# Kernel optimization log

Hardware: AMD Instinct MI355X
Metric: run time of the kernel (lower is better)

## Reference

```python
import jax, jax.numpy as jnp
import numpy as np
import math

EMBED_DIM = 256
NUM_HEADS = 8
FFN_DIM = 1024
EPS = 1e-5


def layer_norm(x, g, b):
    mu = jnp.mean(x, axis=-1, keepdims=True)
    var = jnp.var(x, axis=-1, keepdims=True)
    return (x - mu) / jnp.sqrt(var + EPS) * g + b


def setup_inputs() -> dict:
    key = jax.random.key(0)
    ks = jax.random.split(key, 10)
    B, L, D, F = 4, 2048, EMBED_DIM, FFN_DIM
    x = jax.random.normal(ks[0], (B, L, D), dtype=jnp.float32)
    mask = jnp.ones((B, L), dtype=jnp.int32)
    # FFN params (PyTorch Linear default-ish scale)
    W1 = jax.random.normal(ks[1], (D, F), dtype=jnp.float32) / np.sqrt(D)
    b1 = jnp.zeros((F,), dtype=jnp.float32)
    W2 = jax.random.normal(ks[2], (F, D), dtype=jnp.float32) / np.sqrt(F)
    b2 = jnp.zeros((D,), dtype=jnp.float32)
    g1 = jnp.ones((D,), dtype=jnp.float32)
    be1 = jnp.zeros((D,), dtype=jnp.float32)
    g2 = jnp.ones((D,), dtype=jnp.float32)
    be2 = jnp.zeros((D,), dtype=jnp.float32)
    return {"x": x, "mask": mask, "W1": W1, "b1": b1, "W2": W2, "b2": b2,
            "g1": g1, "be1": be1, "g2": g2, "be2": be2}


def quantum_attention(x, mask):
    B, L, D = x.shape
    H, dk = NUM_HEADS, D // NUM_HEADS
    xh = x.reshape(B, L, H, dk).transpose(0, 2, 1, 3)  # [B,H,L,dk]
    # per-token mean over batch and heads -> [L, dk]
    m = jnp.mean(xh, axis=(0, 1))
    # closed form of the single-qubit RX circuit: P(|1>) = sin^2(angle/2)
    dot = m @ m.T  # [L, L]
    ang = jnp.clip(dot, -math.pi, math.pi)
    scores = jnp.sin(ang * 0.5) ** 2  # [L, L], shared across B and H
    attn = jnp.broadcast_to(scores[None, None], (B, H, L, L))
    attn = jnp.where(mask[:, None, None, :] == 0, -1e9, attn)
    attn = jax.nn.softmax(attn, axis=-1)
    out = jnp.einsum('bhij,bhjd->bhid', attn, xh)  # values are xh itself
    return out.transpose(0, 2, 1, 3).reshape(B, L, D)


def reference(x, mask, W1, b1, W2, b2, g1, be1, g2, be2):
    attn_out = quantum_attention(x, mask)
    h = layer_norm(x + attn_out, g1, be1)
    ffn = jax.nn.relu(h @ W1 + b1) @ W2 + b2
    return layer_norm(h + ffn, g2, be2)
```

## Files before the change

### kernel.cpp

```cpp
#include <hip/hip_runtime.h>
#include <hip/hip_bf16.h>


#define B_ 4
#define L_ 2048
#define D_ 256
#define F_ 1024
#define PI_F 3.14159265358979323846f

typedef __bf16 bf16x8 __attribute__((ext_vector_type(8)));
typedef float floatx4 __attribute__((ext_vector_type(4)));
typedef unsigned short ushortx4 __attribute__((ext_vector_type(4)));

#define WAIT_VM(n) asm volatile("s_waitcnt vmcnt(" #n ")" ::: "memory")
#define SCHED0() __builtin_amdgcn_sched_barrier(0)
#define BARRIER() do { SCHED0(); __builtin_amdgcn_s_barrier(); SCHED0(); } while (0)

__device__ __forceinline__ unsigned short f2bf(float f) {
    unsigned int u = __float_as_uint(f);
    u = (u + 0x7FFFu + ((u >> 16) & 1u)) >> 16;
    return (unsigned short)u;
}
__device__ __forceinline__ float bf2f(unsigned short u) {
    union { unsigned int i; float f; } v; v.i = ((unsigned int)u) << 16; return v.f;
}

__device__ __forceinline__ void async_cp16(unsigned short* lds, const unsigned short* g) {
    __builtin_amdgcn_global_load_lds(
        (const __attribute__((address_space(1))) unsigned int*)g,
        (__attribute__((address_space(3))) unsigned int*)lds, 16, 0, 0);
}

__global__ __launch_bounds__(256) void k_prep(const float* __restrict__ x,
                                              const float* __restrict__ W1,
                                              const float* __restrict__ W2,
                                              const int* __restrict__ mask,
                                              unsigned short* __restrict__ mb,
                                              unsigned short* __restrict__ XmT,
                                              unsigned short* __restrict__ W1T,
                                              unsigned short* __restrict__ W2T) {
    __shared__ float tile[32][33];
    int r = blockIdx.x, t = threadIdx.x;
    if (r >= 2560) {
        int idx = (r - 2560) * 256 + t;
        int l = idx >> 5, k = idx & 31;
        float s = 0.f;
#pragma unroll
        for (int b = 0; b < B_; b++) {
            const float* xp = x + ((size_t)(b * L_ + l)) * D_ + k;
#pragma unroll
            for (int h = 0; h < 8; h++) s += xp[h * 32];
        }
        mb[idx] = f2bf(s * (1.f / 32.f));
        return;
    }
    const float* in; unsigned short* outp; int R, C; const int* mrow = nullptr; size_t bo = 0;
    int bx, by;
    if (r < 2048) {
        int z = r >> 9, rem = r & 511; by = rem >> 3; bx = rem & 7;
        in = x; outp = XmT; R = L_; C = 256; bo = (size_t)z * R * C; mrow = mask + z * L_;
    } else if (r < 2304) {
        int rem = r - 2048; bx = rem & 31; by = rem >> 5;
        in = W1; outp = W1T; R = 256; C = 1024;
    } else {
        int rem = r - 2304; bx = rem & 7; by = rem >> 3;
        in = W2; outp = W2T; R = 1024; C = 256;
    }
    int r0 = by * 32, c0 = bx * 32;
    int tx = t & 31, ty = t >> 5;
#pragma unroll
    for (int rr = 0; rr < 4; rr++) {
        int rw = ty + rr * 8;
        tile[rw][tx] = in[bo + (size_t)(r0 + rw) * C + c0 + tx];
    }
    float mfac = 1.f;
    if (mrow) mfac = mrow[r0 + tx] ? 1.f : 0.f;
    __syncthreads();
#pragma unroll
    for (int rr = 0; rr < 4; rr++) {
        int c = ty + rr * 8;
        outp[bo + (size_t)(c0 + c) * R + r0 + tx] = f2bf(tile[tx][c] * mfac);
    }
}

__global__ __launch_bounds__(256) void k_scores_mfma(const unsigned short* __restrict__ mb,
                                                     const int* __restrict__ mask,
                                                     unsigned short* __restrict__ E,
                                                     float* __restrict__ rowpart) {
    __shared__ float part[128][2][4];
    const int t = threadIdx.x, lane = t & 63, wid = t >> 6;
    const int wm = (wid >> 1) * 64, wn = (wid & 1) * 32;
    const int lr = lane & 15, lq = lane >> 4;
    int m0 = blockIdx.y * 128, n0 = blockIdx.x * 64;
    bf16x8 af[4], bfr[2];
#pragma unroll
    for (int i = 0; i < 4; i++)
        af[i] = *(const bf16x8*)(mb + (size_t)(m0 + wm + i * 16 + lr) * 32 + lq * 8);
#pragma unroll
    for (int j = 0; j < 2; j++)
        bfr[j] = *(const bf16x8*)(mb + (size_t)(n0 + wn + j * 16 + lr) * 32 + lq * 8);
    floatx4 acc[4][2];
#pragma unroll
    for (int i = 0; i < 4; i++)
#pragma unroll
        for (int j = 0; j < 2; j++) {
            acc[i][j] = (floatx4){0.f, 0.f, 0.f, 0.f};
            acc[i][j] = __builtin_amdgcn_mfma_f32_16x16x32_bf16(af[i], bfr[j], acc[i][j], 0, 0, 0);
        }
    float mv[4][2];
#pragma unroll
    for (int b = 0; b < 4; b++) {
        mv[b][0] = mask[b * L_ + n0 + wn + lr] ? 1.f : 0.f;
        mv[b][1] = mask[b * L_ + n0 + wn + 16 + lr] ? 1.f : 0.f;
    }
#pragma unroll
    for (int i = 0; i < 4; i++) {
#pragma unroll
        for (int j = 0; j < 2; j++)
#pragma unroll
            for (int r = 0; r < 4; r++) {
                int row = m0 + wm + i * 16 + lq * 4 + r;
                int col = n0 + wn + j * 16 + lr;
                float d = fminf(fmaxf(acc[i][j][r], -PI_F), PI_F);
                float sn = __sinf(0.5f * d);
                float e = __expf(sn * sn);
                acc[i][j][r] = e;
                E[(size_t)row * L_ + col] = f2bf(e);
            }
#pragma unroll
        for (int r = 0; r < 4; r++) {
            float pb[4];
#pragma unroll
            for (int b = 0; b < 4; b++)
                pb[b] = acc[i][0][r] * mv[b][0] + acc[i][1][r] * mv[b][1];
#pragma unroll
            for (int o = 1; o < 16; o <<= 1)
#pragma unroll
                for (int b = 0; b < 4; b++) pb[b] += __shfl_xor(pb[b], o);
            if (lr == 0) {
                int lrow = wm + i * 16 + lq * 4 + r;
#pragma unroll
                for (int b = 0; b < 4; b++) part[lrow][wid & 1][b] = pb[b];
            }
        }
    }
    __syncthreads();
    if (t < 128) {
        int grow = m0 + t;
#pragma unroll
        for (int b = 0; b < 4; b++)
            rowpart[((size_t)grow * 4 + b) * 32 + blockIdx.x] = part[t][0][b] + part[t][1][b];
    }
}

__global__ __launch_bounds__(256) void k_av(const unsigned short* __restrict__ E,
                                            const unsigned short* __restrict__ XmT,
                                            unsigned short* __restrict__ Cb) {
    __shared__ __align__(16) unsigned short sbuf[3][128 * 64 + 64 * 64];
    const int t = threadIdx.x, lane = t & 63, wid = t >> 6;
    const int wm = (wid >> 1) * 64, wn = (wid & 1) * 32;
    const int lr = lane & 15, lq = lane >> 4;
    const int lrow = lane >> 3, lseg = lane & 7;

    int bid = blockIdx.x;
    int swz = (bid & 7) * 32 + (bid >> 3);
    int m0 = (swz >> 4) * 128, n0 = (swz & 15) * 64;

    const unsigned short* Ag[4]; int sAoff[4];
#pragma unroll
    for (int q = 0; q < 4; q++) {
        int rl = wid * 32 + q * 8 + lrow;
        Ag[q] = E + (size_t)(m0 + rl) * L_ + ((lseg - rl) & 7) * 8;
        sAoff[q] = (wid * 32 + q * 8) * 64;
    }
    const unsigned short* Bg[2]; int sBoff[2];
#pragma unroll
    for (int q = 0; q < 2; q++) {
        int rl = wid * 16 + q * 8 + lrow;
        Bg[q] = XmT + (size_t)(n0 + rl) * L_ + ((lseg - rl) & 7) * 8;
        sBoff[q] = 8192 + (wid * 16 + q * 8) * 64;
    }
    int arot[4], aroff[4], brot[2], broff[2];
#pragma unroll
    for (int i = 0; i < 4; i++) { int ar = wm + i * 16 + lr; aroff[i] = ar * 64; arot[i] = lq + ar; }
#pragma unroll
    for (int j = 0; j < 2; j++) { int br = wn + j * 16 + lr; broff[j] = 8192 + br * 64; brot[j] = lq + br; }

    floatx4 acc[4][2];
#pragma unroll
    for (int i = 0; i < 4; i++)
#pragma unroll
        for (int j = 0; j < 2; j++) acc[i][j] = (floatx4){0.f, 0.f, 0.f, 0.f};

    auto stage = [&](unsigned short* base, int k0) {
#pragma unroll
        for (int q = 0; q < 4; q++) async_cp16(base + sAoff[q], Ag[q] + k0);
#pragma unroll
        for (int q = 0; q < 2; q++) async_cp16(base + sBoff[q], Bg[q] + k0);
    };
    auto compute = [&](const unsigned short* base) {
#pragma unroll
        for (int s = 0; s < 2; s++) {
            bf16x8 af[4], bfr[2];
#pragma unroll
            for (int i = 0; i < 4; i++)
                af[i] = *(const bf16x8*)(base + aroff[i] + ((s * 4 + arot[i]) & 7) * 8);
#pragma unroll
            for (int j = 0; j < 2; j++)
                bfr[j] = *(const bf16x8*)(base + broff[j] + ((s * 4 + brot[j]) & 7) * 8);
#pragma unroll
            for (int i = 0; i < 4; i++)
#pragma unroll
                for (int j = 0; j < 2; j++)
                    acc[i][j] = __builtin_amdgcn_mfma_f32_16x16x32_bf16(af[i], bfr[j], acc[i][j], 0, 0, 0);
        }
    };

    unsigned short *p0 = sbuf[0], *p1 = sbuf[1], *p2 = sbuf[2];
    stage(p0, 0); stage(p1, 64); stage(p2, 128);
    WAIT_VM(12); BARRIER();
    for (int p = 0; p < 29; ++p) {
        compute(p0);
        BARRIER();
        stage(p0, (p + 3) << 6);
        WAIT_VM(12); BARRIER();
        unsigned short* tmp = p0; p0 = p1; p1 = p2; p2 = tmp;
    }
    compute(p0);
    BARRIER();
    WAIT_VM(6); BARRIER();
    compute(p1);
    BARRIER();
    WAIT_VM(0); BARRIER();
    compute(p2);

#pragma unroll
    for (int i = 0; i < 4; i++)
#pragma unroll
        for (int j = 0; j < 2; j++)
#pragma unroll
            for (int r = 0; r < 4; r++) {
                int row = m0 + wm + i * 16 + lq * 4 + r;
                int col = n0 + wn + j * 16 + lr;
                Cb[(size_t)row * 1024 + col] = f2bf(acc[i][j][r]);
            }
}

__global__ __launch_bounds__(256) void k_ln1(const float* __restrict__ x, const unsigned short* __restrict__ Cb,
                                             const float* __restrict__ rowpart,
                                             const float* __restrict__ g_, const float* __restrict__ be_,
                                             unsigned short* __restrict__ hb) {
    int t = threadIdx.x, wid = t >> 6, lane = t & 63;
    int tok = (blockIdx.x << 2) + wid;
    int b = tok >> 11, i = tok & (L_ - 1);
    float rp = rowpart[((size_t)i * 4 + b) * 32 + (lane & 31)];
#pragma unroll
    for (int o = 1; o < 32; o <<= 1) rp += __shfl_xor(rp, o);
    float rs = rp;
    float4 xv = *(const float4*)(x + (size_t)tok * D_ + lane * 4);
    ushortx4 cv = *(const ushortx4*)(Cb + (size_t)i * 1024 + b * 256 + lane * 4);
    float v0 = xv.x + bf2f(cv.x) / rs;
    float v1 = xv.y + bf2f(cv.y) / rs;
    float v2 = xv.z + bf2f(cv.z) / rs;
    float v3 = xv.w + bf2f(cv.w) / rs;
    float s  = v0 + v1 + v2 + v3;
    float s2 = v0 * v0 + v1 * v1 + v2 * v2 + v3 * v3;
#pragma unroll
    for (int o = 1; o < 64; o <<= 1) { s += __shfl_xor(s, o); s2 += __shfl_xor(s2, o); }
    float mu = s * (1.f / 256.f);
    float var = s2 * (1.f / 256.f) - mu * mu;
    float r = rsqrtf(var + 1e-5f);
    float4 gv = *(const float4*)(g_ + lane * 4);
    float4 bv = *(const float4*)(be_ + lane * 4);
    ushortx4 o4;
    o4.x = f2bf((v0 - mu) * r * gv.x + bv.x);
    o4.y = f2bf((v1 - mu) * r * gv.y + bv.y);
    o4.z = f2bf((v2 - mu) * r * gv.z + bv.z);
    o4.w = f2bf((v3 - mu) * r * gv.w + bv.w);
    *(ushortx4*)(hb + (size_t)tok * D_ + lane * 4) = o4;
}

__global__ __launch_bounds__(256) void k_gemm1(const unsigned short* __restrict__ hb,
                                               const unsigned short* __restrict__ W1T,
                                               const float* __restrict__ b1, unsigned short* __restrict__ t1) {
    __shared__ __align__(16) unsigned short sbuf[2][128 * 64 + 128 * 64];
    const int t = threadIdx.x, lane = t & 63, wid = t >> 6;
    const int wm = (wid >> 1) * 64, wn = (wid & 1) * 64;
    const int lr = lane & 15, lq = lane >> 4;
    const int lrow8 = lane >> 3, lseg = lane & 7;

    int bid = blockIdx.x;
    int swz = (bid & 7) * 64 + (bid >> 3);
    int m0 = (swz >> 3) * 128, n0 = (swz & 7) * 128;

    const unsigned short* Ag[4]; const unsigned short* Bg[4]; int aoff[4], boff4[4];
#pragma unroll
    for (int q = 0; q < 4; q++) {
        int rl = q * 32 + wid * 8 + lrow8;
        int seg = (lseg - rl) & 7;
        Ag[q] = hb + (size_t)(m0 + rl) * 256 + seg * 8;
        Bg[q] = W1T + (size_t)(n0 + rl) * 256 + seg * 8;
        aoff[q] = (q * 32 + wid * 8) * 64;
        boff4[q] = 8192 + (q * 32 + wid * 8) * 64;
    }
    int arot[4], aroff[4], brot[4], broff[4];
#pragma unroll
    for (int i = 0; i < 4; i++) { int ar = wm + i * 16 + lr; aroff[i] = ar * 64; arot[i] = lq + ar; }
#pragma unroll
    for (int j = 0; j < 4; j++) { int br = wn + j * 16 + lr; broff[j] = 8192 + br * 64; brot[j] = lq + br; }

    floatx4 acc[4][4];
#pragma unroll
    for (int i = 0; i < 4; i++)
#pragma unroll
        for (int j = 0; j < 4; j++) acc[i][j] = (floatx4){0.f, 0.f, 0.f, 0.f};

    auto stage = [&](unsigned short* base, int k0) {
#pragma unroll
        for (int q = 0; q < 4; q++) { async_cp16(base + aoff[q], Ag[q] + k0); async_cp16(base + boff4[q], Bg[q] + k0); }
    };
    auto compute = [&](const unsigned short* base) {
#pragma unroll
        for (int s = 0; s < 2; s++) {
            bf16x8 af[4], bfr[4];
#pragma unroll
            for (int i = 0; i < 4; i++) af[i] = *(const bf16x8*)(base + aroff[i] + ((s * 4 + arot[i]) & 7) * 8);
#pragma unroll
            for (int j = 0; j < 4; j++) bfr[j] = *(const bf16x8*)(base + broff[j] + ((s * 4 + brot[j]) & 7) * 8);
#pragma unroll
            for (int i = 0; i < 4; i++)
#pragma unroll
                for (int j = 0; j < 4; j++)
                    acc[i][j] = __builtin_amdgcn_mfma_f32_16x16x32_bf16(af[i], bfr[j], acc[i][j], 0, 0, 0);
        }
    };

    unsigned short *pa = sbuf[0], *pb = sbuf[1];
    stage(pa, 0); stage(pb, 64);
    WAIT_VM(8); BARRIER();
    compute(pa);
    BARRIER();
    stage(pa, 128);
    WAIT_VM(8); BARRIER();
    compute(pb);
    BARRIER();
    stage(pb, 192);
    WAIT_VM(8); BARRIER();
    compute(pa);
    BARRIER();
    WAIT_VM(0); BARRIER();
    compute(pb);

    float bb[4];
#pragma unroll
    for (int j = 0; j < 4; j++) bb[j] = b1[n0 + wn + j * 16 + lr];
#pragma unroll
    for (int i = 0; i < 4; i++)
#pragma unroll
        for (int j = 0; j < 4; j++) {
            int col = n0 + wn + j * 16 + lr;
#pragma unroll
            for (int r = 0; r < 4; r++) {
                int row = m0 + wm + i * 16 + lq * 4 + r;
                t1[(size_t)row * 1024 + col] = f2bf(fmaxf(acc[i][j][r] + bb[j], 0.f));
            }
        }
}

__global__ __launch_bounds__(256) void k_gemm2ln(const unsigned short* __restrict__ t1,
                                                 const unsigned short* __restrict__ W2T,
                                                 const float* __restrict__ b2,
                                                 const unsigned short* __restrict__ hb,
                                                 const float* __restrict__ g_, const float* __restrict__ be_,
                                                 float* __restrict__ out) {
    __shared__ __align__(16) unsigned short sbuf[3][32 * 64 + 256 * 64];
    __shared__ float red[4][32][2];
    const int t = threadIdx.x, lane = t & 63, wid = t >> 6;
    const int wn = wid * 64;
    const int lr = lane & 15, lq = lane >> 4;
    const int lrow8 = lane >> 3, lseg = lane & 7;
    int m0 = blockIdx.x * 32;

    int arl = wid * 8 + lrow8;
    const unsigned short* Ag = t1 + (size_t)(m0 + arl) * 1024 + (((lseg - arl) & 7) * 8);
    int sAoff = (wid * 8) * 64;
    const unsigned short* Bg[8]; int sBoff[8];
#pragma unroll
    for (int q = 0; q < 8; q++) {
        int rl = q * 32 + wid * 8 + lrow8;
        Bg[q] = W2T + (size_t)rl * 1024 + (((lseg - rl) & 7) * 8);
        sBoff[q] = 2048 + (q * 32 + wid * 8) * 64;
    }
    int aroff[2], arot[2];
#pragma unroll
    for (int i = 0; i < 2; i++) { int ar = i * 16 + lr; aroff[i] = ar * 64; arot[i] = lq + ar; }
    int brot[4], broff[4];
#pragma unroll
    for (int j = 0; j < 4; j++) { int br = wn + j * 16 + lr; broff[j] = 2048 + br * 64; brot[j] = lq + br; }

    floatx4 acc[2][4];
#pragma unroll
    for (int i = 0; i < 2; i++)
#pragma unroll
        for (int j = 0; j < 4; j++) acc[i][j] = (floatx4){0.f, 0.f, 0.f, 0.f};

    auto stage = [&](unsigned short* base, int k0) {
        async_cp16(base + sAoff, Ag + k0);
#pragma unroll
        for (int q = 0; q < 8; q++) async_cp16(base + sBoff[q], Bg[q] + k0);
    };
    auto compute = [&](const unsigned short* base) {
#pragma unroll
        for (int s = 0; s < 2; s++) {
            bf16x8 af[2];
#pragma unroll
            for (int i = 0; i < 2; i++)
                af[i] = *(const bf16x8*)(base + aroff[i] + ((s * 4 + arot[i]) & 7) * 8);
#pragma unroll
            for (int j = 0; j < 4; j++) {
                bf16x8 bfr = *(const bf16x8*)(base + broff[j] + ((s * 4 + brot[j]) & 7) * 8);
#pragma unroll
                for (int i = 0; i < 2; i++)
                    acc[i][j] = __builtin_amdgcn_mfma_f32_16x16x32_bf16(af[i], bfr, acc[i][j], 0, 0, 0);
            }
        }
    };

    unsigned short *p0 = sbuf[0], *p1 = sbuf[1], *p2 = sbuf[2];
    stage(p0, 0); stage(p1, 64); stage(p2, 128);
    WAIT_VM(18); BARRIER();
    for (int p = 0; p < 13; ++p) {
        compute(p0);
        BARRIER();
        stage(p0, (p + 3) << 6);
        WAIT_VM(18); BARRIER();
        unsigned short* tmp = p0; p0 = p1; p1 = p2; p2 = tmp;
    }
    compute(p0);
    BARRIER();
    WAIT_VM(9); BARRIER();
    compute(p1);
    BARRIER();
    WAIT_VM(0); BARRIER();
    compute(p2);

    float psum[2][4], psq[2][4];
#pragma unroll
    for (int i = 0; i < 2; i++)
#pragma unroll
        for (int r = 0; r < 4; r++) { psum[i][r] = 0.f; psq[i][r] = 0.f; }
#pragma unroll
    for (int i = 0; i < 2; i++)
#pragma unroll
        for (int j = 0; j < 4; j++) {
            int col = wn + j * 16 + lr;
            float bv = b2[col];
#pragma unroll
            for (int r = 0; r < 4; r++) {
                int row = m0 + i * 16 + lq * 4 + r;
                float v = acc[i][j][r] + bv + bf2f(hb[(size_t)row * 256 + col]);
                acc[i][j][r] = v;
                psum[i][r] += v; psq[i][r] += v * v;
            }
        }
#pragma unroll
    for (int o = 1; o < 16; o <<= 1)
#pragma unroll
        for (int i = 0; i < 2; i++)
#pragma unroll
            for (int r = 0; r < 4; r++) { psum[i][r] += __shfl_xor(psum[i][r], o); psq[i][r] += __shfl_xor(psq[i][r], o); }
    if (lr == 0) {
#pragma unroll
        for (int i = 0; i < 2; i++)
#pragma unroll
            for (int r = 0; r < 4; r++) {
                int lrow = i * 16 + lq * 4 + r;
                red[wid][lrow][0] = psum[i][r];
                red[wid][lrow][1] = psq[i][r];
            }
    }
    __syncthreads();
#pragma unroll
    for (int i = 0; i < 2; i++)
#pragma unroll
        for (int r = 0; r < 4; r++) {
            int lrow = i * 16 + lq * 4 + r;
            float s  = red[0][lrow][0] + red[1][lrow][0] + red[2][lrow][0] + red[3][lrow][0];
            float s2 = red[0][lrow][1] + red[1][lrow][1] + red[2][lrow][1] + red[3][lrow][1];
            float mu = s * (1.f / 256.f);
            float var = s2 * (1.f / 256.f) - mu * mu;
            float rc = rsqrtf(var + 1e-5f);
            int row = m0 + lrow;
#pragma unroll
            for (int j = 0; j < 4; j++) {
                int col = wn + j * 16 + lr;
                out[(size_t)row * 256 + col] = (acc[i][j][r] - mu) * rc * g_[col] + be_[col];
            }
        }
}

extern "C" void kernel_launch(void* const* d_in, const int* in_sizes, int n_in,
                              void* d_out, int out_size, void* d_ws, size_t ws_size,
                              hipStream_t stream) {
    const float* x   = (const float*)d_in[0];
    const int*  mask = (const int*)d_in[1];
    const float* W1  = (const float*)d_in[2];
    const float* b1  = (const float*)d_in[3];
    const float* W2  = (const float*)d_in[4];
    const float* b2  = (const float*)d_in[5];
    const float* g1  = (const float*)d_in[6];
    const float* be1 = (const float*)d_in[7];
    const float* g2  = (const float*)d_in[8];
    const float* be2 = (const float*)d_in[9];
    float* out = (float*)d_out;

    char* w = (char*)d_ws;
    unsigned short* mb_   = (unsigned short*)w;  w += 65536 * 2;
    unsigned short* E_    = (unsigned short*)w;  w += (size_t)L_ * L_ * 2;
    unsigned short* XmT_  = (unsigned short*)w;  w += (size_t)1024 * L_ * 2;
    unsigned short* W1T_  = (unsigned short*)w;  w += 262144 * 2;
    unsigned short* W2T_  = (unsigned short*)w;  w += 262144 * 2;
    unsigned short* Cb_   = (unsigned short*)w;  w += (size_t)L_ * 1024 * 2;
    unsigned short* hb_   = (unsigned short*)w;  w += (size_t)8192 * 256 * 2;
    unsigned short* t1_   = (unsigned short*)w;  w += (size_t)8192 * 1024 * 2;
    float*          rp_   = (float*)w;           w += (size_t)2048 * 4 * 32 * 4;

    k_prep<<<2816, 256, 0, stream>>>(x, W1, W2, mask, mb_, XmT_, W1T_, W2T_);
    k_scores_mfma<<<dim3(32, 16), 256, 0, stream>>>(mb_, mask, E_, rp_);
    k_av<<<256, 256, 0, stream>>>(E_, XmT_, Cb_);
    k_ln1<<<2048, 256, 0, stream>>>(x, Cb_, rp_, g1, be1, hb_);
    k_gemm1<<<512, 256, 0, stream>>>(hb_, W1T_, b1, t1_);
    k_gemm2ln<<<256, 256, 0, stream>>>(t1_, W2T_, b2, hb_, g2, be2, out);
}
```

Measured before the change: 143.2 us.

## Compute softmax row sums via extra mask columns in the AV GEMM

Appends 0/1 mask rows per batch to the transposed value matrix, so the AV GEMM also produces the masked exp row sums as extra output columns. This removes the shuffle reduction, shared-memory partials and rowpart buffer from the scores kernel, and the 32-way reduction in LN1. The cost is a 17th column tile in the AV GEMM (272 blocks instead of 256). The denominator is now rounded to bf16, which slightly reduces precision.

```diff
diff --git a/kernel.cpp b/kernel.cpp
--- a/kernel.cpp
+++ b/kernel.cpp
@@ -42,16 +42,25 @@
     __shared__ float tile[32][33];
     int r = blockIdx.x, t = threadIdx.x;
     if (r >= 2560) {
-        int idx = (r - 2560) * 256 + t;
-        int l = idx >> 5, k = idx & 31;
-        float s = 0.f;
-#pragma unroll
-        for (int b = 0; b < B_; b++) {
-            const float* xp = x + ((size_t)(b * L_ + l)) * D_ + k;
-#pragma unroll
-            for (int h = 0; h < 8; h++) s += xp[h * 32];
-        }
-        mb[idx] = f2bf(s * (1.f / 32.f));
+        if (r < 2816) {
+            int idx = (r - 2560) * 256 + t;
+            int l = idx >> 5, k = idx & 31;
+            float s = 0.f;
+#pragma unroll
+            for (int b = 0; b < B_; b++) {
+                const float* xp = x + ((size_t)(b * L_ + l)) * D_ + k;
+#pragma unroll
+                for (int h = 0; h < 8; h++) s += xp[h * 32];
+            }
+            mb[idx] = f2bf(s * (1.f / 32.f));
+        } else {
+#pragma unroll
+            for (int c = 0; c < 32; c++) {
+                int e = c * 256 + t;
+                int b = e >> 11, j = e & (L_ - 1);
+                XmT[(size_t)(1024 + b) * L_ + j] = mask[b * L_ + j] ? 0x3F80 : 0;
+            }
+        }
         return;
     }
     const float* in; unsigned short* outp; int R, C; const int* mrow = nullptr; size_t bo = 0;
@@ -84,10 +93,7 @@
 }
 
 __global__ __launch_bounds__(256) void k_scores_mfma(const unsigned short* __restrict__ mb,
-                                                     const int* __restrict__ mask,
-                                                     unsigned short* __restrict__ E,
-                                                     float* __restrict__ rowpart) {
-    __shared__ float part[128][2][4];
+                                                     unsigned short* __restrict__ E) {
     const int t = threadIdx.x, lane = t & 63, wid = t >> 6;
     const int wm = (wid >> 1) * 64, wn = (wid & 1) * 32;
     const int lr = lane & 15, lq = lane >> 4;
@@ -107,14 +113,8 @@
             acc[i][j] = (floatx4){0.f, 0.f, 0.f, 0.f};
             acc[i][j] = __builtin_amdgcn_mfma_f32_16x16x32_bf16(af[i], bfr[j], acc[i][j], 0, 0, 0);
         }
-    float mv[4][2];
-#pragma unroll
-    for (int b = 0; b < 4; b++) {
-        mv[b][0] = mask[b * L_ + n0 + wn + lr] ? 1.f : 0.f;
-        mv[b][1] = mask[b * L_ + n0 + wn + 16 + lr] ? 1.f : 0.f;
-    }
-#pragma unroll
-    for (int i = 0; i < 4; i++) {
+#pragma unroll
+    for (int i = 0; i < 4; i++)
 #pragma unroll
         for (int j = 0; j < 2; j++)
 #pragma unroll
@@ -123,34 +123,8 @@
                 int col = n0 + wn + j * 16 + lr;
                 float d = fminf(fmaxf(acc[i][j][r], -PI_F), PI_F);
                 float sn = __sinf(0.5f * d);
-                float e = __expf(sn * sn);
-                acc[i][j][r] = e;
-                E[(size_t)row * L_ + col] = f2bf(e);
-            }
-#pragma unroll
-        for (int r = 0; r < 4; r++) {
-            float pb[4];
-#pragma unroll
-            for (int b = 0; b < 4; b++)
-                pb[b] = acc[i][0][r] * mv[b][0] + acc[i][1][r] * mv[b][1];
-#pragma unroll
-            for (int o = 1; o < 16; o <<= 1)
-#pragma unroll
-                for (int b = 0; b < 4; b++) pb[b] += __shfl_xor(pb[b], o);
-            if (lr == 0) {
-                int lrow = wm + i * 16 + lq * 4 + r;
-#pragma unroll
-                for (int b = 0; b < 4; b++) part[lrow][wid & 1][b] = pb[b];
-            }
-        }
-    }
-    __syncthreads();
-    if (t < 128) {
-        int grow = m0 + t;
-#pragma unroll
-        for (int b = 0; b < 4; b++)
-            rowpart[((size_t)grow * 4 + b) * 32 + blockIdx.x] = part[t][0][b] + part[t][1][b];
-    }
+                E[(size_t)row * L_ + col] = f2bf(__expf(sn * sn));
+            }
 }
 
 __global__ __launch_bounds__(256) void k_av(const unsigned short* __restrict__ E,
@@ -163,8 +137,8 @@
     const int lrow = lane >> 3, lseg = lane & 7;
 
     int bid = blockIdx.x;
-    int swz = (bid & 7) * 32 + (bid >> 3);
-    int m0 = (swz >> 4) * 128, n0 = (swz & 15) * 64;
+    int swz = (bid & 7) * 34 + (bid >> 3);
+    int m0 = (swz / 17) * 128, n0 = (swz % 17) * 64;
 
     const unsigned short* Ag[4]; int sAoff[4];
 #pragma unroll
@@ -242,23 +216,19 @@
             for (int r = 0; r < 4; r++) {
                 int row = m0 + wm + i * 16 + lq * 4 + r;
                 int col = n0 + wn + j * 16 + lr;
-                Cb[(size_t)row * 1024 + col] = f2bf(acc[i][j][r]);
+                Cb[(size_t)row * 1088 + col] = f2bf(acc[i][j][r]);
             }
 }
 
 __global__ __launch_bounds__(256) void k_ln1(const float* __restrict__ x, const unsigned short* __restrict__ Cb,
-                                             const float* __restrict__ rowpart,
                                              const float* __restrict__ g_, const float* __restrict__ be_,
                                              unsigned short* __restrict__ hb) {
     int t = threadIdx.x, wid = t >> 6, lane = t & 63;
     int tok = (blockIdx.x << 2) + wid;
     int b = tok >> 11, i = tok & (L_ - 1);
-    float rp = rowpart[((size_t)i * 4 + b) * 32 + (lane & 31)];
-#pragma unroll
-    for (int o = 1; o < 32; o <<= 1) rp += __shfl_xor(rp, o);
-    float rs = rp;
+    float rs = bf2f(Cb[(size_t)i * 1088 + 1024 + b]);
     float4 xv = *(const float4*)(x + (size_t)tok * D_ + lane * 4);
-    ushortx4 cv = *(const ushortx4*)(Cb + (size_t)i * 1024 + b * 256 + lane * 4);
+    ushortx4 cv = *(const ushortx4*)(Cb + (size_t)i * 1088 + b * 256 + lane * 4);
     float v0 = xv.x + bf2f(cv.x) / rs;
     float v1 = xv.y + bf2f(cv.y) / rs;
     float v2 = xv.z + bf2f(cv.z) / rs;
@@ -517,18 +487,17 @@
     char* w = (char*)d_ws;
     unsigned short* mb_   = (unsigned short*)w;  w += 65536 * 2;
     unsigned short* E_    = (unsigned short*)w;  w += (size_t)L_ * L_ * 2;
-    unsigned short* XmT_  = (unsigned short*)w;  w += (size_t)1024 * L_ * 2;
+    unsigned short* XmT_  = (unsigned short*)w;  w += (size_t)1088 * L_ * 2;
     unsigned short* W1T_  = (unsigned short*)w;  w += 262144 * 2;
     unsigned short* W2T_  = (unsigned short*)w;  w += 262144 * 2;
-    unsigned short* Cb_   = (unsigned short*)w;  w += (size_t)L_ * 1024 * 2;
+    unsigned short* Cb_   = (unsigned short*)w;  w += (size_t)L_ * 1088 * 2;
     unsigned short* hb_   = (unsigned short*)w;  w += (size_t)8192 * 256 * 2;
     unsigned short* t1_   = (unsigned short*)w;  w += (size_t)8192 * 1024 * 2;
-    float*          rp_   = (float*)w;           w += (size_t)2048 * 4 * 32 * 4;
-
-    k_prep<<<2816, 256, 0, stream>>>(x, W1, W2, mask, mb_, XmT_, W1T_, W2T_);
-    k_scores_mfma<<<dim3(32, 16), 256, 0, stream>>>(mb_, mask, E_, rp_);
-    k_av<<<256, 256, 0, stream>>>(E_, XmT_, Cb_);
-    k_ln1<<<2048, 256, 0, stream>>>(x, Cb_, rp_, g1, be1, hb_);
+
+    k_prep<<<2817, 256, 0, stream>>>(x, W1, W2, mask, mb_, XmT_, W1T_, W2T_);
+    k_scores_mfma<<<dim3(32, 16), 256, 0, stream>>>(mb_, E_);
+    k_av<<<272, 256, 0, stream>>>(E_, XmT_, Cb_);
+    k_ln1<<<2048, 256, 0, stream>>>(x, Cb_, g1, be1, hb_);
     k_gemm1<<<512, 256, 0, stream>>>(hb_, W1T_, b1, t1_);
     k_gemm2ln<<<256, 256, 0, stream>>>(t1_, W2T_, b2, hb_, g2, be2, out);
 }
```

After: 137.5 us. 1.04x faster.
